# Optimization experiments

Measured on AMD Instinct MI355X. Metric: run time of the kernel, lower is better.

## Reference

```python
import jax, jax.numpy as jnp
import numpy as np

SCALE = 0.125  # 1/sqrt(d_head=64)

def setup_inputs() -> dict:
    key = jax.random.key(0)
    kq, kk, kv = jax.random.split(key, 3)
    B, S, D = 16, 2048, 64
    q = jax.random.normal(kq, (B, S, D), dtype=jnp.float32)
    k = jax.random.normal(kk, (B, S, D), dtype=jnp.float32)
    v = jax.random.normal(kv, (B, S, D), dtype=jnp.float32)
    return {"q": q, "k": k, "v": v}

def reference(q, k, v):
    # scores: [B, S, S] = q @ k^T * scale
    scores = jnp.einsum('bqd,bkd->bqk', q, k) * SCALE
    attention = jax.nn.softmax(scores, axis=2)
    # dropout p=0.0 -> identity (eval); attn_mask=None -> no masking
    context = jnp.einsum('bqk,bkd->bqd', attention, v)
    return (context, attention)
```

## Files before the change

### kernel.cpp

```cpp
#include <hip/hip_runtime.h>

#define BB 16
#define SS 2048
#define DD 64
#define L2E 1.44269504f
#define A3C 4.32808512f

typedef _Float16 half8 __attribute__((ext_vector_type(8)));
typedef _Float16 half4 __attribute__((ext_vector_type(4)));
typedef float f32x4 __attribute__((ext_vector_type(4)));

typedef const __attribute__((address_space(1))) void* gas_ptr;
typedef __attribute__((address_space(3))) void* las_ptr;

#define TILE_SYNC(N)                                            \
  do {                                                          \
    asm volatile("s_waitcnt vmcnt(" #N ")" ::: "memory");       \
    __builtin_amdgcn_s_barrier();                               \
    __builtin_amdgcn_sched_barrier(0);                          \
  } while (0)

__global__ __launch_bounds__(256) void setup_kernel(const float* __restrict__ K,
                                                    const float* __restrict__ V,
                                                    _Float16* __restrict__ Kh,
                                                    _Float16* __restrict__ VT) {
  __shared__ float tile[64][65];
  int b = blockIdx.x >> 5, kt = blockIdx.x & 31;
  int tid = threadIdx.x;
  size_t base = ((size_t)b * SS + (size_t)kt * 64) * DD;
  const float4* Kq = (const float4*)(K + base);
  const float4* Vq = (const float4*)(V + base);
  half4* Khq = (half4*)(Kh + base);
#pragma unroll
  for (int it = 0; it < 4; ++it) {
    int i = tid + it * 256;
    float4 kv = Kq[i];
    half4 h;
    h[0] = (_Float16)kv.x; h[1] = (_Float16)kv.y;
    h[2] = (_Float16)kv.z; h[3] = (_Float16)kv.w;
    Khq[i] = h;
    float4 vv = Vq[i];
    int row = i >> 4, c4 = (i & 15) << 2;
    tile[row][c4 + 0] = vv.x; tile[row][c4 + 1] = vv.y;
    tile[row][c4 + 2] = vv.z; tile[row][c4 + 3] = vv.w;
  }
  __syncthreads();
  int d = tid >> 2, seg = tid & 3;
  half8 o0, o1;
#pragma unroll
  for (int j = 0; j < 8; ++j) o0[j] = (_Float16)tile[seg * 16 + j][d];
#pragma unroll
  for (int j = 0; j < 8; ++j) o1[j] = (_Float16)tile[seg * 16 + 8 + j][d];
  _Float16* dst = VT + ((size_t)b * DD + d) * SS + (size_t)kt * 64 + seg * 16;
  *(half8*)dst = o0;
  *(half8*)(dst + 8) = o1;
}

__device__ __forceinline__ void stage64(const _Float16* __restrict__ gbase, size_t rstride,
                                        _Float16* lds, int tid) {
  int w = tid >> 6, lam = tid & 63;
#pragma unroll
  for (int a = 0; a < 2; ++a) {
    int rloc = lam >> 3;
    int r = w * 16 + a * 8 + rloc;
    int byt = ((lam & 7) * 16) ^ (rloc << 4);
    const _Float16* g = gbase + (size_t)r * rstride + (byt >> 1);
    _Float16* lp = lds + (w * 16 + a * 8) * 64;
    __builtin_amdgcn_global_load_lds((gas_ptr)g, (las_ptr)lp, 16, 0, 0);
  }
}

__device__ __forceinline__ void load_qfrag(const float* __restrict__ Qp,
                                           half8& qa0, half8& qa1) {
  float4 v0 = *(const float4*)(Qp);
  float4 v1 = *(const float4*)(Qp + 4);
  float4 v2 = *(const float4*)(Qp + 32);
  float4 v3 = *(const float4*)(Qp + 36);
  qa0[0] = (_Float16)(v0.x * 0.125f); qa0[1] = (_Float16)(v0.y * 0.125f);
  qa0[2] = (_Float16)(v0.z * 0.125f); qa0[3] = (_Float16)(v0.w * 0.125f);
  qa0[4] = (_Float16)(v1.x * 0.125f); qa0[5] = (_Float16)(v1.y * 0.125f);
  qa0[6] = (_Float16)(v1.z * 0.125f); qa0[7] = (_Float16)(v1.w * 0.125f);
  qa1[0] = (_Float16)(v2.x * 0.125f); qa1[1] = (_Float16)(v2.y * 0.125f);
  qa1[2] = (_Float16)(v2.z * 0.125f); qa1[3] = (_Float16)(v2.w * 0.125f);
  qa1[4] = (_Float16)(v3.x * 0.125f); qa1[5] = (_Float16)(v3.y * 0.125f);
  qa1[6] = (_Float16)(v3.z * 0.125f); qa1[7] = (_Float16)(v3.w * 0.125f);
}

__global__ __launch_bounds__(256, 2) void attn_kernel(const float* __restrict__ Q,
                                                      const _Float16* __restrict__ Kh,
                                                      const _Float16* __restrict__ VT,
                                                      float* __restrict__ ctx_out,
                                                      float* __restrict__ attn_out) {
  __shared__ __attribute__((aligned(16))) _Float16 Kl[3][64 * 64];
  __shared__ __attribute__((aligned(16))) _Float16 Vl[3][64 * 64];

  int tid = threadIdx.x;
  int w = tid >> 6, l = tid & 63, g = l >> 4, c = l & 15;
  int bid = (int)blockIdx.x;
  int remap = (bid & 7) * 64 + (bid >> 3);
  int b = remap >> 5, qb = remap & 31;
  size_t qr = (size_t)b * SS + (size_t)qb * 64 + (size_t)w * 16;
  const _Float16* KB = Kh + (size_t)b * SS * DD;
  const _Float16* VB = VT + (size_t)b * DD * SS;
  int swz = (c & 7) << 4;

  stage64(KB, DD, Kl[0], tid);
  stage64(KB + (size_t)64 * DD, DD, Kl[1], tid);

  half8 qa0, qa1;
  load_qfrag(Q + (qr + c) * DD + 8 * g, qa0, qa1);

  float lsum = 0.f;
  int bufc = 0, bufs = 2;
  for (int t = 0; t < 32; ++t) {
    if (t < 31) TILE_SYNC(2); else TILE_SYNC(0);
    if (t + 2 < 32) stage64(KB + (size_t)(t + 2) * 64 * DD, DD, Kl[bufs], tid);
#pragma unroll
    for (int kt = 0; kt < 4; ++kt) {
      const _Float16* kb = &Kl[bufc][(kt * 16 + c) * 64];
      half8 kf0 = *(const half8*)(kb + (((16 * g) ^ swz) >> 1));
      half8 kf1 = *(const half8*)(kb + (((64 + 16 * g) ^ swz) >> 1));
      f32x4 s = {0.f, 0.f, 0.f, 0.f};
      s = __builtin_amdgcn_mfma_f32_16x16x32_f16(kf0, qa0, s, 0, 0, 0);
      s = __builtin_amdgcn_mfma_f32_16x16x32_f16(kf1, qa1, s, 0, 0, 0);
      lsum += exp2f(fmaf(s[0], L2E, -A3C)) + exp2f(fmaf(s[1], L2E, -A3C)) +
              exp2f(fmaf(s[2], L2E, -A3C)) + exp2f(fmaf(s[3], L2E, -A3C));
    }
    bufc = (bufc == 2) ? 0 : bufc + 1;
    bufs = (bufs == 2) ? 0 : bufs + 1;
  }
  lsum += __shfl_xor(lsum, 16);
  lsum += __shfl_xor(lsum, 32);
  float ac = -__log2f(lsum) - A3C;

  __syncthreads();

  stage64(KB, DD, Kl[0], tid);
  stage64(VB, SS, Vl[0], tid);
  stage64(KB + (size_t)64 * DD, DD, Kl[1], tid);
  stage64(VB + 64, SS, Vl[1], tid);

  f32x4 cacc[4] = {{0.f, 0.f, 0.f, 0.f}, {0.f, 0.f, 0.f, 0.f},
                   {0.f, 0.f, 0.f, 0.f}, {0.f, 0.f, 0.f, 0.f}};
  bufc = 0; bufs = 2;
  for (int t = 0; t < 32; ++t) {
    if (t == 0) TILE_SYNC(4);
    else if (t == 1) TILE_SYNC(8);
    else if (t < 31) TILE_SYNC(12);
    else TILE_SYNC(8);
    if (t + 2 < 32) {
      stage64(KB + (size_t)(t + 2) * 64 * DD, DD, Kl[bufs], tid);
      stage64(VB + (size_t)(t + 2) * 64, SS, Vl[bufs], tid);
    }
#pragma unroll
    for (int kt = 0; kt < 4; ++kt) {
      const _Float16* kb = &Kl[bufc][(kt * 16 + c) * 64];
      half8 kf0 = *(const half8*)(kb + (((16 * g) ^ swz) >> 1));
      half8 kf1 = *(const half8*)(kb + (((64 + 16 * g) ^ swz) >> 1));
      f32x4 s = {0.f, 0.f, 0.f, 0.f};
      s = __builtin_amdgcn_mfma_f32_16x16x32_f16(kf0, qa0, s, 0, 0, 0);
      s = __builtin_amdgcn_mfma_f32_16x16x32_f16(kf1, qa1, s, 0, 0, 0);

      float p0 = exp2f(fmaf(s[0], L2E, ac));
      float p1 = exp2f(fmaf(s[1], L2E, ac));
      float p2 = exp2f(fmaf(s[2], L2E, ac));
      float p3 = exp2f(fmaf(s[3], L2E, ac));
      float4 st = {p0, p1, p2, p3};
      *(float4*)(attn_out + (qr + c) * SS + t * 64 + kt * 16 + 4 * g) = st;

      half4 pf;
      pf[0] = (_Float16)p0; pf[1] = (_Float16)p1;
      pf[2] = (_Float16)p2; pf[3] = (_Float16)p3;
#pragma unroll
      for (int dt = 0; dt < 4; ++dt) {
        const _Float16* vb = &Vl[bufc][(dt * 16 + c) * 64];
        half4 vf = *(const half4*)(vb + (((32 * kt + 8 * g) ^ swz) >> 1));
        cacc[dt] = __builtin_amdgcn_mfma_f32_16x16x16f16(pf, vf, cacc[dt], 0, 0, 0);
      }
    }
    bufc = (bufc == 2) ? 0 : bufc + 1;
    bufs = (bufs == 2) ? 0 : bufs + 1;
  }

#pragma unroll
  for (int dt = 0; dt < 4; ++dt)
#pragma unroll
    for (int j = 0; j < 4; ++j)
      ctx_out[(qr + 4 * g + j) * DD + dt * 16 + c] = cacc[dt][j];
}

extern "C" void kernel_launch(void* const* d_in, const int* in_sizes, int n_in,
                              void* d_out, int out_size, void* d_ws, size_t ws_size,
                              hipStream_t stream) {
  const float* q = (const float*)d_in[0];
  const float* k = (const float*)d_in[1];
  const float* v = (const float*)d_in[2];
  float* ctx = (float*)d_out;
  float* attn = ctx + (size_t)BB * SS * DD;
  _Float16* Kh = (_Float16*)d_ws;
  _Float16* VT = Kh + (size_t)BB * SS * DD;
  setup_kernel<<<dim3(BB * 32), dim3(256), 0, stream>>>(k, v, Kh, VT);
  attn_kernel<<<dim3(BB * 32), dim3(256), 0, stream>>>(q, Kh, VT, ctx, attn);
}
```

Baseline: 95.65 us.

## Give each wave private K/V staging buffers and drop block-wide barriers

```diff
diff --git a/kernel.cpp b/kernel.cpp
--- a/kernel.cpp
+++ b/kernel.cpp
@@ -13,10 +13,9 @@
 typedef const __attribute__((address_space(1))) void* gas_ptr;
 typedef __attribute__((address_space(3))) void* las_ptr;
 
-#define TILE_SYNC(N)                                            \
+#define WAITV(N)                                                \
   do {                                                          \
     asm volatile("s_waitcnt vmcnt(" #N ")" ::: "memory");       \
-    __builtin_amdgcn_s_barrier();                               \
     __builtin_amdgcn_sched_barrier(0);                          \
   } while (0)
 
@@ -56,17 +55,27 @@
   *(half8*)(dst + 8) = o1;
 }
 
-__device__ __forceinline__ void stage64(const _Float16* __restrict__ gbase, size_t rstride,
-                                        _Float16* lds, int tid) {
-  int w = tid >> 6, lam = tid & 63;
-#pragma unroll
-  for (int a = 0; a < 2; ++a) {
+__device__ __forceinline__ void stageK32(const _Float16* __restrict__ kb,
+                                         _Float16* lds, int lam) {
+#pragma unroll
+  for (int a = 0; a < 4; ++a) {
     int rloc = lam >> 3;
-    int r = w * 16 + a * 8 + rloc;
+    int r = a * 8 + rloc;
     int byt = ((lam & 7) * 16) ^ (rloc << 4);
-    const _Float16* g = gbase + (size_t)r * rstride + (byt >> 1);
-    _Float16* lp = lds + (w * 16 + a * 8) * 64;
-    __builtin_amdgcn_global_load_lds((gas_ptr)g, (las_ptr)lp, 16, 0, 0);
+    __builtin_amdgcn_global_load_lds((gas_ptr)(kb + (size_t)r * DD + (byt >> 1)),
+                                     (las_ptr)(lds + a * 512), 16, 0, 0);
+  }
+}
+
+__device__ __forceinline__ void stageV32(const _Float16* __restrict__ vb,
+                                         _Float16* lds, int lam) {
+#pragma unroll
+  for (int a = 0; a < 4; ++a) {
+    int kt = a >> 1;
+    int d = (a & 1) * 32 + (lam >> 1);
+    int h = lam & 1;
+    __builtin_amdgcn_global_load_lds((gas_ptr)(vb + (size_t)d * SS + kt * 16 + h * 8),
+                                     (las_ptr)(lds + a * 512), 16, 0, 0);
   }
 }
 
@@ -91,8 +100,7 @@
                                                       const _Float16* __restrict__ VT,
                                                       float* __restrict__ ctx_out,
                                                       float* __restrict__ attn_out) {
-  __shared__ __attribute__((aligned(16))) _Float16 Kl[3][64 * 64];
-  __shared__ __attribute__((aligned(16))) _Float16 Vl[3][64 * 64];
+  __shared__ __attribute__((aligned(16))) _Float16 buf[4][4][2048];
 
   int tid = threadIdx.x;
   int w = tid >> 6, l = tid & 63, g = l >> 4, c = l & 15;
@@ -102,61 +110,60 @@
   size_t qr = (size_t)b * SS + (size_t)qb * 64 + (size_t)w * 16;
   const _Float16* KB = Kh + (size_t)b * SS * DD;
   const _Float16* VB = VT + (size_t)b * DD * SS;
+  _Float16* WB = &buf[w][0][0];
   int swz = (c & 7) << 4;
-
-  stage64(KB, DD, Kl[0], tid);
-  stage64(KB + (size_t)64 * DD, DD, Kl[1], tid);
 
   half8 qa0, qa1;
   load_qfrag(Q + (qr + c) * DD + 8 * g, qa0, qa1);
 
+  stageK32(KB, WB, l);
+  stageK32(KB + (size_t)32 * DD, WB + 2048, l);
+  stageK32(KB + (size_t)64 * DD, WB + 2 * 2048, l);
+
   float lsum = 0.f;
-  int bufc = 0, bufs = 2;
-  for (int t = 0; t < 32; ++t) {
-    if (t < 31) TILE_SYNC(2); else TILE_SYNC(0);
-    if (t + 2 < 32) stage64(KB + (size_t)(t + 2) * 64 * DD, DD, Kl[bufs], tid);
-#pragma unroll
-    for (int kt = 0; kt < 4; ++kt) {
-      const _Float16* kb = &Kl[bufc][(kt * 16 + c) * 64];
-      half8 kf0 = *(const half8*)(kb + (((16 * g) ^ swz) >> 1));
-      half8 kf1 = *(const half8*)(kb + (((64 + 16 * g) ^ swz) >> 1));
+  for (int t = 0; t < 64; ++t) {
+    if (t < 62) WAITV(8);
+    else if (t == 62) WAITV(4);
+    else WAITV(0);
+    const _Float16* kl = WB + (t & 3) * 2048;
+#pragma unroll
+    for (int kt = 0; kt < 2; ++kt) {
+      const _Float16* kb2 = kl + (kt * 16 + c) * 64;
+      half8 kf0 = *(const half8*)(kb2 + (((16 * g) ^ swz) >> 1));
+      half8 kf1 = *(const half8*)(kb2 + (((64 + 16 * g) ^ swz) >> 1));
       f32x4 s = {0.f, 0.f, 0.f, 0.f};
       s = __builtin_amdgcn_mfma_f32_16x16x32_f16(kf0, qa0, s, 0, 0, 0);
       s = __builtin_amdgcn_mfma_f32_16x16x32_f16(kf1, qa1, s, 0, 0, 0);
       lsum += exp2f(fmaf(s[0], L2E, -A3C)) + exp2f(fmaf(s[1], L2E, -A3C)) +
               exp2f(fmaf(s[2], L2E, -A3C)) + exp2f(fmaf(s[3], L2E, -A3C));
     }
-    bufc = (bufc == 2) ? 0 : bufc + 1;
-    bufs = (bufs == 2) ? 0 : bufs + 1;
+    if (t < 61) {
+      __builtin_amdgcn_sched_barrier(0);
+      stageK32(KB + (size_t)(t + 3) * 32 * DD, WB + ((t + 3) & 3) * 2048, l);
+    }
   }
   lsum += __shfl_xor(lsum, 16);
   lsum += __shfl_xor(lsum, 32);
   float ac = -__log2f(lsum) - A3C;
 
-  __syncthreads();
-
-  stage64(KB, DD, Kl[0], tid);
-  stage64(VB, SS, Vl[0], tid);
-  stage64(KB + (size_t)64 * DD, DD, Kl[1], tid);
-  stage64(VB + 64, SS, Vl[1], tid);
+  stageK32(KB, WB, l);
+  stageV32(VB, WB + 2 * 2048, l);
+  stageK32(KB + (size_t)32 * DD, WB + 2048, l);
+  stageV32(VB + 32, WB + 3 * 2048, l);
 
   f32x4 cacc[4] = {{0.f, 0.f, 0.f, 0.f}, {0.f, 0.f, 0.f, 0.f},
                    {0.f, 0.f, 0.f, 0.f}, {0.f, 0.f, 0.f, 0.f}};
-  bufc = 0; bufs = 2;
-  for (int t = 0; t < 32; ++t) {
-    if (t == 0) TILE_SYNC(4);
-    else if (t == 1) TILE_SYNC(8);
-    else if (t < 31) TILE_SYNC(12);
-    else TILE_SYNC(8);
-    if (t + 2 < 32) {
-      stage64(KB + (size_t)(t + 2) * 64 * DD, DD, Kl[bufs], tid);
-      stage64(VB + (size_t)(t + 2) * 64, SS, Vl[bufs], tid);
-    }
-#pragma unroll
-    for (int kt = 0; kt < 4; ++kt) {
-      const _Float16* kb = &Kl[bufc][(kt * 16 + c) * 64];
-      half8 kf0 = *(const half8*)(kb + (((16 * g) ^ swz) >> 1));
-      half8 kf1 = *(const half8*)(kb + (((64 + 16 * g) ^ swz) >> 1));
+  for (int t = 0; t < 64; ++t) {
+    if (t == 0) WAITV(8);
+    else if (t < 63) WAITV(10);
+    else WAITV(2);
+    const _Float16* kl = WB + (t & 1) * 2048;
+    const _Float16* vl = WB + (2 + (t & 1)) * 2048;
+#pragma unroll
+    for (int kt = 0; kt < 2; ++kt) {
+      const _Float16* kb2 = kl + (kt * 16 + c) * 64;
+      half8 kf0 = *(const half8*)(kb2 + (((16 * g) ^ swz) >> 1));
+      half8 kf1 = *(const half8*)(kb2 + (((64 + 16 * g) ^ swz) >> 1));
       f32x4 s = {0.f, 0.f, 0.f, 0.f};
       s = __builtin_amdgcn_mfma_f32_16x16x32_f16(kf0, qa0, s, 0, 0, 0);
       s = __builtin_amdgcn_mfma_f32_16x16x32_f16(kf1, qa1, s, 0, 0, 0);
@@ -166,20 +173,22 @@
       float p2 = exp2f(fmaf(s[2], L2E, ac));
       float p3 = exp2f(fmaf(s[3], L2E, ac));
       float4 st = {p0, p1, p2, p3};
-      *(float4*)(attn_out + (qr + c) * SS + t * 64 + kt * 16 + 4 * g) = st;
+      *(float4*)(attn_out + (qr + c) * SS + t * 32 + kt * 16 + 4 * g) = st;
 
       half4 pf;
       pf[0] = (_Float16)p0; pf[1] = (_Float16)p1;
       pf[2] = (_Float16)p2; pf[3] = (_Float16)p3;
 #pragma unroll
       for (int dt = 0; dt < 4; ++dt) {
-        const _Float16* vb = &Vl[bufc][(dt * 16 + c) * 64];
-        half4 vf = *(const half4*)(vb + (((32 * kt + 8 * g) ^ swz) >> 1));
+        half4 vf = *(const half4*)(vl + kt * 1024 + (dt * 16 + c) * 16 + 4 * g);
         cacc[dt] = __builtin_amdgcn_mfma_f32_16x16x16f16(pf, vf, cacc[dt], 0, 0, 0);
       }
     }
-    bufc = (bufc == 2) ? 0 : bufc + 1;
-    bufs = (bufs == 2) ? 0 : bufs + 1;
+    if (t < 62) {
+      __builtin_amdgcn_sched_barrier(0);
+      stageK32(KB + (size_t)(t + 2) * 32 * DD, WB + ((t + 2) & 1) * 2048, l);
+      stageV32(VB + (size_t)(t + 2) * 32, WB + (2 + ((t + 2) & 1)) * 2048, l);
+    }
   }
 
 #pragma unroll
```

Measured after the change: 114.9 us. 20.2% more time.
